# Kernel optimization log

Measured on AMD Instinct MI355X. Metric: run time of the kernel, lower is better.

Reference implementation:

```python
import jax, jax.numpy as jnp
import numpy as np

LEVELS = [5023, 1256, 314, 79, 20]  # mesh vertex counts, fine -> coarse
T = 64        # number of audio frames
LATENT = 128  # latent_channels
S = 9         # spiral length
OUT_CH = [32, 64, 64, 128]


def setup_inputs() -> dict:
    key = jax.random.key(0)
    ks = list(jax.random.split(key, 40))
    nk = lambda: ks.pop()
    inp = {}
    inp["latent"] = jax.random.normal(nk(), (T, LATENT), jnp.float32)
    inp["actor"] = jax.random.normal(nk(), (LEVELS[0], 3), jnp.float32)
    # spiral indices per mesh level (levels 0..3 carry SpiralConvs)
    for l in range(4):
        n = LEVELS[l]
        inp[f"spiral{l}"] = jax.random.randint(nk(), (n, S), 0, n)
    # sparse up-transforms: level l+1 (coarse) -> level l (fine), ~3 nnz per fine vertex
    for l in range(4):
        nf, nc = LEVELS[l], LEVELS[l + 1]
        nnz = 3 * nf
        inp[f"up{l}_rows"] = jax.random.randint(nk(), (nnz,), 0, nf)
        inp[f"up{l}_cols"] = jax.random.randint(nk(), (nnz,), 0, nc)
        inp[f"up{l}_vals"] = jax.random.uniform(nk(), (nnz,), jnp.float32)
    def lin(k, od, idim):
        scale = np.sqrt(2.0 / (od + idim)).astype(np.float32)  # xavier-uniform-ish std
        return jax.random.normal(k, (od, idim), jnp.float32) * scale
    # de_layers[0]: Linear(latent -> num_vert * out_channels[-1])
    inp["W0"] = lin(nk(), LEVELS[4] * OUT_CH[-1], LATENT)
    inp["b0"] = jnp.zeros((LEVELS[4] * OUT_CH[-1],), jnp.float32)
    # SpiralDeblock convs (coarse -> fine): 128->128, 128->64, 64->64, 64->32
    inp["W1"] = lin(nk(), 128, 128 * S); inp["b1"] = jnp.zeros((128,), jnp.float32)
    inp["W2"] = lin(nk(), 64, 128 * S);  inp["b2"] = jnp.zeros((64,), jnp.float32)
    inp["W3"] = lin(nk(), 64, 64 * S);   inp["b3"] = jnp.zeros((64,), jnp.float32)
    inp["W4"] = lin(nk(), 32, 64 * S);   inp["b4"] = jnp.zeros((32,), jnp.float32)
    # final SpiralConv 32 -> 3 (init=True in torch zeros it; use small randn for testing)
    inp["Wf"] = lin(nk(), 3, 32 * S) * 0.1
    inp["bf"] = jnp.zeros((3,), jnp.float32)
    return inp


def spiral_conv(x, idx, W, b):
    # x: [T, n_in, C]; idx: [n, S] -> gather spiral neighborhoods, flatten, linear
    t, n = x.shape[0], idx.shape[0]
    g = x[:, idx.reshape(-1), :].reshape(t, n, -1)  # [T, n, S*C]
    return g @ W.T + b


def pool(x, rows, cols, vals, n_out):
    # sparse up-transform: out[:, rows] += x[:, cols] * vals  (scatter-add)
    g = x[:, cols, :] * vals[None, :, None]  # [T, nnz, C]
    return jnp.zeros((x.shape[0], n_out, x.shape[2]), x.dtype).at[:, rows].add(g)


def reference(latent, actor, spiral0, spiral1, spiral2, spiral3,
              up0_rows, up0_cols, up0_vals, up1_rows, up1_cols, up1_vals,
              up2_rows, up2_cols, up2_vals, up3_rows, up3_cols, up3_vals,
              W0, b0, W1, b1, W2, b2, W3, b3, W4, b4, Wf, bf):
    t = latent.shape[0]
    x = (latent @ W0.T + b0).reshape(t, LEVELS[4], OUT_CH[-1])  # [T, 20, 128]
    x = jax.nn.elu(spiral_conv(pool(x, up3_rows, up3_cols, up3_vals, LEVELS[3]), spiral3, W1, b1))
    x = jax.nn.elu(spiral_conv(pool(x, up2_rows, up2_cols, up2_vals, LEVELS[2]), spiral2, W2, b2))
    x = jax.nn.elu(spiral_conv(pool(x, up1_rows, up1_cols, up1_vals, LEVELS[1]), spiral1, W3, b3))
    x = jax.nn.elu(spiral_conv(pool(x, up0_rows, up0_cols, up0_vals, LEVELS[0]), spiral0, W4, b4))
    x = spiral_conv(x, spiral0, Wf, bf)  # [T, 5023, 3]
    return x + actor[None]  # per-frame offsets added to neutral actor mesh
```

## Files before the change

kernel.cpp:

```cpp
#include <hip/hip_runtime.h>
#include <hip/hip_bf16.h>

#define T_FRAMES 64

typedef __bf16 bf16x8 __attribute__((ext_vector_type(8)));
typedef float f32x4 __attribute__((ext_vector_type(4)));

#define NNZ0 15069
#define NNZ1 3768
#define NNZ2 942
#define NNZ3 237
#define N0 5023
#define N1 1256
#define N2 314
#define N3 79
#define N4 20

__global__ __launch_bounds__(256) void linear0_kernel(
    const float* __restrict__ latent, const float* __restrict__ W0,
    const float* __restrict__ b0, __bf16* __restrict__ out) {
  int id = blockIdx.x * 256 + threadIdx.x;
  if (id >= 64 * 2560) return;
  int j = id % 2560;
  int t = id / 2560;
  const float* lrow = latent + t * 128;
  const float* wrow = W0 + j * 128;
  float acc = b0[j];
#pragma unroll 8
  for (int k = 0; k < 128; ++k) acc = fmaf(lrow[k], wrow[k], acc);
  out[id] = (__bf16)acc;
}

__global__ __launch_bounds__(256) void cvt_all_kernel(
    const float* __restrict__ W1, const float* __restrict__ W2,
    const float* __restrict__ W3, const float* __restrict__ W4,
    const float* __restrict__ Wf, __bf16* __restrict__ o) {
  int i = blockIdx.x * 256 + threadIdx.x;
  if (i < 147456) { o[i] = (__bf16)W1[i]; return; }
  if (i < 221184) { o[i] = (__bf16)W2[i - 147456]; return; }
  if (i < 258048) { o[i] = (__bf16)W3[i - 221184]; return; }
  if (i < 276480) { o[i] = (__bf16)W4[i - 258048]; return; }
  if (i < 281088) {
    int j = i - 276480;
    o[i] = (j / 288 < 3) ? (__bf16)Wf[j] : (__bf16)0.f;
  }
}

__global__ __launch_bounds__(256) void csr_count_kernel(
    const int* __restrict__ r0, const int* __restrict__ r1,
    const int* __restrict__ r2, const int* __restrict__ r3,
    int* __restrict__ c0, int* __restrict__ c1,
    int* __restrict__ c2, int* __restrict__ c3) {
  int i = blockIdx.x * 256 + threadIdx.x;
  if (i < NNZ0) atomicAdd(&c0[r0[i]], 1);
  else if (i < NNZ0 + NNZ1) atomicAdd(&c1[r1[i - NNZ0]], 1);
  else if (i < NNZ0 + NNZ1 + NNZ2) atomicAdd(&c2[r2[i - NNZ0 - NNZ1]], 1);
  else if (i < NNZ0 + NNZ1 + NNZ2 + NNZ3) atomicAdd(&c3[r3[i - NNZ0 - NNZ1 - NNZ2]], 1);
}

__global__ __launch_bounds__(256) void csr_scan_kernel(
    const int* __restrict__ c0, const int* __restrict__ c1,
    const int* __restrict__ c2, const int* __restrict__ c3,
    int* __restrict__ o0, int* __restrict__ o1,
    int* __restrict__ o2, int* __restrict__ o3,
    int* __restrict__ u0, int* __restrict__ u1,
    int* __restrict__ u2, int* __restrict__ u3) {
  const int b = blockIdx.x;
  const int* counts = b == 0 ? c0 : b == 1 ? c1 : b == 2 ? c2 : c3;
  int* off = b == 0 ? o0 : b == 1 ? o1 : b == 2 ? o2 : o3;
  int* cur = b == 0 ? u0 : b == 1 ? u1 : b == 2 ? u2 : u3;
  const int n = b == 0 ? N0 : b == 1 ? N1 : b == 2 ? N2 : N3;

  __shared__ int part[256];
  const int chunk = (n + 255) / 256;
  const int start = threadIdx.x * chunk;
  const int end = min(start + chunk, n);
  int s = 0;
  for (int i = start; i < end; ++i) s += counts[i];
  part[threadIdx.x] = s;
  __syncthreads();
  for (int d = 1; d < 256; d <<= 1) {
    int v = (threadIdx.x >= d) ? part[threadIdx.x - d] : 0;
    __syncthreads();
    part[threadIdx.x] += v;
    __syncthreads();
  }
  int run = (threadIdx.x == 0) ? 0 : part[threadIdx.x - 1];
  for (int i = start; i < end; ++i) {
    off[i] = run;
    cur[i] = run;
    run += counts[i];
  }
  if (threadIdx.x == 255) off[n] = run;
}

__global__ __launch_bounds__(256) void csr_bucket_kernel(
    const int* __restrict__ r0, const int* __restrict__ r1,
    const int* __restrict__ r2, const int* __restrict__ r3,
    const int* __restrict__ q0, const int* __restrict__ q1,
    const int* __restrict__ q2, const int* __restrict__ q3,
    const float* __restrict__ v0, const float* __restrict__ v1,
    const float* __restrict__ v2, const float* __restrict__ v3,
    int* __restrict__ u0, int* __restrict__ u1,
    int* __restrict__ u2, int* __restrict__ u3,
    int2* __restrict__ p0, int2* __restrict__ p1,
    int2* __restrict__ p2, int2* __restrict__ p3) {
  int i = blockIdx.x * 256 + threadIdx.x;
  if (i < NNZ0) {
    int p = atomicAdd(&u0[r0[i]], 1);
    p0[p] = make_int2(q0[i], __float_as_int(v0[i]));
  } else if (i < NNZ0 + NNZ1) {
    int e = i - NNZ0;
    int p = atomicAdd(&u1[r1[e]], 1);
    p1[p] = make_int2(q1[e], __float_as_int(v1[e]));
  } else if (i < NNZ0 + NNZ1 + NNZ2) {
    int e = i - NNZ0 - NNZ1;
    int p = atomicAdd(&u2[r2[e]], 1);
    p2[p] = make_int2(q2[e], __float_as_int(v2[e]));
  } else if (i < NNZ0 + NNZ1 + NNZ2 + NNZ3) {
    int e = i - NNZ0 - NNZ1 - NNZ2;
    int p = atomicAdd(&u3[r3[e]], 1);
    p3[p] = make_int2(q3[e], __float_as_int(v3[e]));
  }
}

template <int C, int TT>
__global__ __launch_bounds__(256) void pool_csr_kernel(
    const __bf16* __restrict__ x, const int* __restrict__ off,
    const int2* __restrict__ pk, __bf16* __restrict__ out,
    int n_in, int n_out) {
  unsigned id = blockIdx.x * 256u + threadIdx.x;
  unsigned total = (unsigned)n_out * (T_FRAMES / TT) * C;
  if (id >= total) return;
  const int c = id % C;
  const unsigned rt = id / C;
  const int row = rt % n_out;
  const int tb = rt / n_out;

  const int o0 = off[row], o1 = off[row + 1];
  float acc[TT];
#pragma unroll
  for (int u = 0; u < TT; ++u) acc[u] = 0.f;

  for (int j = o0; j < o1; ++j) {
    const int2 rec = pk[j];
    const float val = __int_as_float(rec.y);
    const __bf16* xp = x + ((size_t)(tb * TT) * n_in + rec.x) * C + c;
#pragma unroll
    for (int u = 0; u < TT; ++u)
      acc[u] = fmaf(val, (float)xp[(size_t)u * n_in * C], acc[u]);
  }

#pragma unroll
  for (int u = 0; u < TT; ++u)
    out[((size_t)(tb * TT + u) * n_out + row) * C + c] = (__bf16)acc[u];
}

template <int CIN, int COUT>
__global__ __launch_bounds__(256) void conv_mfma_kernel(
    const __bf16* __restrict__ x, const int* __restrict__ idx,
    const __bf16* __restrict__ Wb, const float* __restrict__ bias,
    __bf16* __restrict__ out, int n) {
  constexpr int K = 9 * CIN;
  constexpr int KK = K / 32;
  constexpr int NT = COUT / 16;

  const int lane = threadIdx.x & 63;
  const int wid = threadIdx.x >> 6;
  const int mtile = blockIdx.x * 4 + wid;
  const int col = lane & 15;
  const int kg = lane >> 4;

  const int m = mtile * 16 + col;
  const int t = m / n;
  const int v = m - t * n;

  int base[9];
#pragma unroll
  for (int s = 0; s < 9; ++s) base[s] = (t * n + idx[v * 9 + s]) * CIN;

  f32x4 acc[NT];
#pragma unroll
  for (int nt = 0; nt < NT; ++nt) {
    float b = bias[nt * 16 + col];
    acc[nt] = (f32x4){b, b, b, b};
  }

#pragma unroll
  for (int kk = 0; kk < KK; ++kk) {
    const int s = (kk * 32) / CIN;
    const int ci0 = (kk * 32) % CIN;
    bf16x8 a = *(const bf16x8*)(x + base[s] + ci0 + kg * 8);
#pragma unroll
    for (int nt = 0; nt < NT; ++nt) {
      bf16x8 bfr = *(const bf16x8*)(Wb + (size_t)(nt * 16 + col) * K + kk * 32 + kg * 8);
      acc[nt] = __builtin_amdgcn_mfma_f32_16x16x32_bf16(a, bfr, acc[nt], 0, 0, 0);
    }
  }

#pragma unroll
  for (int j = 0; j < 4; ++j) {
    const int mr = mtile * 16 + kg * 4 + j;
#pragma unroll
    for (int nt = 0; nt < NT; ++nt) {
      float aa = acc[nt][j];
      aa = aa > 0.f ? aa : expm1f(aa);
      out[(size_t)mr * COUT + nt * 16 + col] = (__bf16)aa;
    }
  }
}

__global__ __launch_bounds__(256) void final_mfma_kernel(
    const __bf16* __restrict__ x, const int* __restrict__ idx,
    const __bf16* __restrict__ Wfp, const float* __restrict__ bf3,
    const float* __restrict__ actor, float* __restrict__ out) {
  constexpr int n = N0;
  const int lane = threadIdx.x & 63;
  const int wid = threadIdx.x >> 6;
  const int mtile = blockIdx.x * 4 + wid;
  const int col = lane & 15;
  const int kg = lane >> 4;

  const int m = mtile * 16 + col;
  const int t = m / n;
  const int v = m - t * n;

  int base[9];
#pragma unroll
  for (int s = 0; s < 9; ++s) base[s] = (t * n + idx[v * 9 + s]) * 32;

  float b = (col < 3) ? bf3[col] : 0.f;
  f32x4 acc = (f32x4){b, b, b, b};

#pragma unroll
  for (int kk = 0; kk < 9; ++kk) {
    bf16x8 a = *(const bf16x8*)(x + base[kk] + kg * 8);
    bf16x8 w = *(const bf16x8*)(Wfp + col * 288 + kk * 32 + kg * 8);
    acc = __builtin_amdgcn_mfma_f32_16x16x32_bf16(a, w, acc, 0, 0, 0);
  }

  if (col < 3) {
#pragma unroll
    for (int j = 0; j < 4; ++j) {
      const int mr = mtile * 16 + kg * 4 + j;
      const int vr = mr % n;
      out[(size_t)mr * 3 + col] = acc[j] + actor[vr * 3 + col];
    }
  }
}

extern "C" void kernel_launch(void* const* d_in, const int* in_sizes, int n_in_args,
                              void* d_out, int out_size, void* d_ws, size_t ws_size,
                              hipStream_t stream) {
  const float* latent = (const float*)d_in[0];
  const float* actor  = (const float*)d_in[1];
  const int* spiral0 = (const int*)d_in[2];
  const int* spiral1 = (const int*)d_in[3];
  const int* spiral2 = (const int*)d_in[4];
  const int* spiral3 = (const int*)d_in[5];
  const int* up0_rows = (const int*)d_in[6];
  const int* up0_cols = (const int*)d_in[7];
  const float* up0_vals = (const float*)d_in[8];
  const int* up1_rows = (const int*)d_in[9];
  const int* up1_cols = (const int*)d_in[10];
  const float* up1_vals = (const float*)d_in[11];
  const int* up2_rows = (const int*)d_in[12];
  const int* up2_cols = (const int*)d_in[13];
  const float* up2_vals = (const float*)d_in[14];
  const int* up3_rows = (const int*)d_in[15];
  const int* up3_cols = (const int*)d_in[16];
  const float* up3_vals = (const float*)d_in[17];
  const float* W0 = (const float*)d_in[18];
  const float* b0 = (const float*)d_in[19];
  const float* W1 = (const float*)d_in[20];
  const float* b1 = (const float*)d_in[21];
  const float* W2 = (const float*)d_in[22];
  const float* b2 = (const float*)d_in[23];
  const float* W3 = (const float*)d_in[24];
  const float* b3 = (const float*)d_in[25];
  const float* W4 = (const float*)d_in[26];
  const float* b4 = (const float*)d_in[27];
  const float* Wf = (const float*)d_in[28];
  const float* bf3 = (const float*)d_in[29];
  float* out = (float*)d_out;

  __bf16* poolbuf = (__bf16*)d_ws;
  __bf16* convout = poolbuf + 20574208;
  __bf16* wbuf = convout + 10287104;
  __bf16* W1b = wbuf;
  __bf16* W2b = W1b + 147456;
  __bf16* W3b = W2b + 73728;
  __bf16* W4b = W3b + 36864;
  __bf16* Wfp = W4b + 18432;
  int* csr = (int*)(wbuf + 281088);
  int* cnt0 = csr;            int* cnt1 = cnt0 + N0;   int* cnt2 = cnt1 + N1;   int* cnt3 = cnt2 + N2;
  int* off0 = csr + 6672;     int* off1 = off0 + N0+1; int* off2 = off1 + N1+1; int* off3 = off2 + N2+1;
  int* cur0 = csr + 13348;    int* cur1 = cur0 + N0;   int* cur2 = cur1 + N1;   int* cur3 = cur2 + N2;
  int2* pk0 = (int2*)(csr + 20020);
  int2* pk1 = pk0 + NNZ0;
  int2* pk2 = pk1 + NNZ1;
  int2* pk3 = pk2 + NNZ2;

  hipMemsetAsync(cnt0, 0, 6672 * sizeof(int), stream);
  csr_count_kernel<<<(20016 + 255) / 256, 256, 0, stream>>>(
      up0_rows, up1_rows, up2_rows, up3_rows, cnt0, cnt1, cnt2, cnt3);
  csr_scan_kernel<<<4, 256, 0, stream>>>(cnt0, cnt1, cnt2, cnt3,
                                         off0, off1, off2, off3,
                                         cur0, cur1, cur2, cur3);
  csr_bucket_kernel<<<(20016 + 255) / 256, 256, 0, stream>>>(
      up0_rows, up1_rows, up2_rows, up3_rows,
      up0_cols, up1_cols, up2_cols, up3_cols,
      up0_vals, up1_vals, up2_vals, up3_vals,
      cur0, cur1, cur2, cur3, pk0, pk1, pk2, pk3);

  cvt_all_kernel<<<(281088 + 255) / 256, 256, 0, stream>>>(W1, W2, W3, W4, Wf, wbuf);

  linear0_kernel<<<(64 * 2560 + 255) / 256, 256, 0, stream>>>(latent, W0, b0, convout);

  pool_csr_kernel<128, 16><<<(N3 * 4 * 128 + 255) / 256, 256, 0, stream>>>(
      convout, off3, pk3, poolbuf, N4, N3);
  conv_mfma_kernel<128, 128><<<N3, 256, 0, stream>>>(poolbuf, spiral3, W1b, b1, convout, N3);

  pool_csr_kernel<128, 16><<<(N2 * 4 * 128 + 255) / 256, 256, 0, stream>>>(
      convout, off2, pk2, poolbuf, N3, N2);
  conv_mfma_kernel<128, 64><<<N2, 256, 0, stream>>>(poolbuf, spiral2, W2b, b2, convout, N2);

  pool_csr_kernel<64, 16><<<(N1 * 4 * 64 + 255) / 256, 256, 0, stream>>>(
      convout, off1, pk1, poolbuf, N2, N1);
  conv_mfma_kernel<64, 64><<<N1, 256, 0, stream>>>(poolbuf, spiral1, W3b, b3, convout, N1);

  pool_csr_kernel<64, 16><<<(N0 * 4 * 64 + 255) / 256, 256, 0, stream>>>(
      convout, off0, pk0, poolbuf, N1, N0);
  conv_mfma_kernel<64, 32><<<N0, 256, 0, stream>>>(poolbuf, spiral0, W4b, b4, convout, N0);

  final_mfma_kernel<<<N0, 256, 0, stream>>>(convout, spiral0, Wfp, bf3, actor, out);
}
```

Before: 480.6 us.

## Switch activations to vertex-major [V,T,C] layout across pool and conv kernels

Activations are now stored vertex-major with all 64 frames of a vertex contiguous, instead of frame-major. The spiral gathers and sparse pool reads then fetch one contiguous 64xC slab per neighbour vertex, which should improve cache-line use and locality for the random-index gathers. Conv kernels are relaunched with one block per vertex, and the small levels use 64-thread blocks over a 2D grid. Small levels get many tiny blocks and the final output is written strided by vertex.

```diff
diff --git a/kernel.cpp b/kernel.cpp
--- a/kernel.cpp
+++ b/kernel.cpp
@@ -15,6 +15,7 @@
 #define N2 314
 #define N3 79
 #define N4 20
+
 
 __global__ __launch_bounds__(256) void linear0_kernel(
     const float* __restrict__ latent, const float* __restrict__ W0,
@@ -28,7 +29,7 @@
   float acc = b0[j];
 #pragma unroll 8
   for (int k = 0; k < 128; ++k) acc = fmaf(lrow[k], wrow[k], acc);
-  out[id] = (__bf16)acc;
+  out[((size_t)(j >> 7) * 64 + t) * 128 + (j & 127)] = (__bf16)acc;
 }
 
 __global__ __launch_bounds__(256) void cvt_all_kernel(
@@ -127,15 +128,14 @@
 template <int C, int TT>
 __global__ __launch_bounds__(256) void pool_csr_kernel(
     const __bf16* __restrict__ x, const int* __restrict__ off,
-    const int2* __restrict__ pk, __bf16* __restrict__ out,
-    int n_in, int n_out) {
+    const int2* __restrict__ pk, __bf16* __restrict__ out, int n_out) {
   unsigned id = blockIdx.x * 256u + threadIdx.x;
   unsigned total = (unsigned)n_out * (T_FRAMES / TT) * C;
   if (id >= total) return;
   const int c = id % C;
   const unsigned rt = id / C;
-  const int row = rt % n_out;
-  const int tb = rt / n_out;
+  const int tb = rt % (T_FRAMES / TT);
+  const int row = rt / (T_FRAMES / TT);
 
   const int o0 = off[row], o1 = off[row + 1];
   float acc[TT];
@@ -145,39 +145,38 @@
   for (int j = o0; j < o1; ++j) {
     const int2 rec = pk[j];
     const float val = __int_as_float(rec.y);
-    const __bf16* xp = x + ((size_t)(tb * TT) * n_in + rec.x) * C + c;
+    const __bf16* xp = x + ((size_t)rec.x * T_FRAMES + tb * TT) * C + c;
 #pragma unroll
     for (int u = 0; u < TT; ++u)
-      acc[u] = fmaf(val, (float)xp[(size_t)u * n_in * C], acc[u]);
-  }
-
-#pragma unroll
-  for (int u = 0; u < TT; ++u)
-    out[((size_t)(tb * TT + u) * n_out + row) * C + c] = (__bf16)acc[u];
-}
-
-template <int CIN, int COUT>
+      acc[u] = fmaf(val, (float)xp[(size_t)u * C], acc[u]);
+  }
+
+  __bf16* op = out + ((size_t)row * T_FRAMES + tb * TT) * C + c;
+#pragma unroll
+  for (int u = 0; u < TT; ++u) op[(size_t)u * C] = (__bf16)acc[u];
+}
+
+template <int CIN, int COUT, int WV>
 __global__ __launch_bounds__(256) void conv_mfma_kernel(
     const __bf16* __restrict__ x, const int* __restrict__ idx,
     const __bf16* __restrict__ Wb, const float* __restrict__ bias,
-    __bf16* __restrict__ out, int n) {
+    __bf16* __restrict__ out) {
   constexpr int K = 9 * CIN;
   constexpr int KK = K / 32;
   constexpr int NT = COUT / 16;
 
   const int lane = threadIdx.x & 63;
   const int wid = threadIdx.x >> 6;
-  const int mtile = blockIdx.x * 4 + wid;
+  const int v = blockIdx.x;
+  const int tq = blockIdx.y * WV + wid;
   const int col = lane & 15;
   const int kg = lane >> 4;
-
-  const int m = mtile * 16 + col;
-  const int t = m / n;
-  const int v = m - t * n;
-
-  int base[9];
-#pragma unroll
-  for (int s = 0; s < 9; ++s) base[s] = (t * n + idx[v * 9 + s]) * CIN;
+  const int trow = tq * 16 + col;
+
+  size_t base[9];
+#pragma unroll
+  for (int s = 0; s < 9; ++s)
+    base[s] = (size_t)idx[v * 9 + s] * (T_FRAMES * CIN) + (size_t)trow * CIN;
 
   f32x4 acc[NT];
 #pragma unroll
@@ -200,12 +199,12 @@
 
 #pragma unroll
   for (int j = 0; j < 4; ++j) {
-    const int mr = mtile * 16 + kg * 4 + j;
+    const size_t tr = tq * 16 + kg * 4 + j;
 #pragma unroll
     for (int nt = 0; nt < NT; ++nt) {
       float aa = acc[nt][j];
       aa = aa > 0.f ? aa : expm1f(aa);
-      out[(size_t)mr * COUT + nt * 16 + col] = (__bf16)aa;
+      out[((size_t)v * T_FRAMES + tr) * COUT + nt * 16 + col] = (__bf16)aa;
     }
   }
 }
@@ -214,20 +213,17 @@
     const __bf16* __restrict__ x, const int* __restrict__ idx,
     const __bf16* __restrict__ Wfp, const float* __restrict__ bf3,
     const float* __restrict__ actor, float* __restrict__ out) {
-  constexpr int n = N0;
   const int lane = threadIdx.x & 63;
   const int wid = threadIdx.x >> 6;
-  const int mtile = blockIdx.x * 4 + wid;
+  const int v = blockIdx.x;
   const int col = lane & 15;
   const int kg = lane >> 4;
-
-  const int m = mtile * 16 + col;
-  const int t = m / n;
-  const int v = m - t * n;
-
-  int base[9];
-#pragma unroll
-  for (int s = 0; s < 9; ++s) base[s] = (t * n + idx[v * 9 + s]) * 32;
+  const int trow = wid * 16 + col;
+
+  size_t base[9];
+#pragma unroll
+  for (int s = 0; s < 9; ++s)
+    base[s] = (size_t)idx[v * 9 + s] * (T_FRAMES * 32) + (size_t)trow * 32;
 
   float b = (col < 3) ? bf3[col] : 0.f;
   f32x4 acc = (f32x4){b, b, b, b};
@@ -240,11 +236,11 @@
   }
 
   if (col < 3) {
+    const float av = actor[v * 3 + col];
 #pragma unroll
     for (int j = 0; j < 4; ++j) {
-      const int mr = mtile * 16 + kg * 4 + j;
-      const int vr = mr % n;
-      out[(size_t)mr * 3 + col] = acc[j] + actor[vr * 3 + col];
+      const int tr = wid * 16 + kg * 4 + j;
+      out[((size_t)tr * N0 + v) * 3 + col] = acc[j] + av;
     }
   }
 }
@@ -318,20 +314,24 @@
   linear0_kernel<<<(64 * 2560 + 255) / 256, 256, 0, stream>>>(latent, W0, b0, convout);
 
   pool_csr_kernel<128, 16><<<(N3 * 4 * 128 + 255) / 256, 256, 0, stream>>>(
-      convout, off3, pk3, poolbuf, N4, N3);
-  conv_mfma_kernel<128, 128><<<N3, 256, 0, stream>>>(poolbuf, spiral3, W1b, b1, convout, N3);
+      convout, off3, pk3, poolbuf, N3);
+  conv_mfma_kernel<128, 128, 1><<<dim3(N3, 4), 64, 0, stream>>>(
+      poolbuf, spiral3, W1b, b1, convout);
 
   pool_csr_kernel<128, 16><<<(N2 * 4 * 128 + 255) / 256, 256, 0, stream>>>(
-      convout, off2, pk2, poolbuf, N3, N2);
-  conv_mfma_kernel<128, 64><<<N2, 256, 0, stream>>>(poolbuf, spiral2, W2b, b2, convout, N2);
+      convout, off2, pk2, poolbuf, N2);
+  conv_mfma_kernel<128, 64, 1><<<dim3(N2, 4), 64, 0, stream>>>(
+      poolbuf, spiral2, W2b, b2, convout);
 
   pool_csr_kernel<64, 16><<<(N1 * 4 * 64 + 255) / 256, 256, 0, stream>>>(
-      convout, off1, pk1, poolbuf, N2, N1);
-  conv_mfma_kernel<64, 64><<<N1, 256, 0, stream>>>(poolbuf, spiral1, W3b, b3, convout, N1);
+      convout, off1, pk1, poolbuf, N1);
+  conv_mfma_kernel<64, 64, 4><<<dim3(N1, 1), 256, 0, stream>>>(
+      poolbuf, spiral1, W3b, b3, convout);
 
   pool_csr_kernel<64, 16><<<(N0 * 4 * 64 + 255) / 256, 256, 0, stream>>>(
-      convout, off0, pk0, poolbuf, N1, N0);
-  conv_mfma_kernel<64, 32><<<N0, 256, 0, stream>>>(poolbuf, spiral0, W4b, b4, convout, N0);
+      convout, off0, pk0, poolbuf, N0);
+  conv_mfma_kernel<64, 32, 4><<<dim3(N0, 1), 256, 0, stream>>>(
+      poolbuf, spiral0, W4b, b4, convout);
 
   final_mfma_kernel<<<N0, 256, 0, stream>>>(convout, spiral0, Wfp, bf3, actor, out);
 }
```

New measurement: 458.3 us. -4.6%, faster.
